# Performance work log

Measured on AMD Instinct MI355X. Metric: run time of the kernel, lower is better.

## Reference

```python
import jax, jax.numpy as jnp
import numpy as np

SLOPE = 0.2  # LeakyReLU negative slope

def _mlp2(x, w1, b1, w2, b2):
    h = jax.nn.leaky_relu(x @ w1 + b1, SLOPE)
    return h @ w2 + b2

def setup_inputs() -> dict:
    key = jax.random.key(0)
    ks = jax.random.split(key, 16)
    B, N, T, A, H = 8, 512, 8, 16, 64
    D = T * A  # node_dim * timestep = 128
    s = 0.1
    return {
        "nodes": jax.random.normal(ks[0], (B, N, T, A), dtype=jnp.float32),
        "edges": jax.random.randint(ks[1], (B, N, N), 0, 2),
        "self_w1": jax.random.normal(ks[2], (D, H), dtype=jnp.float32) * s,
        "self_b1": jnp.zeros((H,), jnp.float32),
        "self_w2": jax.random.normal(ks[3], (H, H), dtype=jnp.float32) * s,
        "self_b2": jnp.zeros((H,), jnp.float32),
        "nb_w1": jax.random.normal(ks[4], (D, H), dtype=jnp.float32) * s,
        "nb_b1": jnp.zeros((H,), jnp.float32),
        "nb_w2": jax.random.normal(ks[5], (H, H), dtype=jnp.float32) * s,
        "nb_b2": jnp.zeros((H,), jnp.float32),
        "comb_w1": jax.random.normal(ks[6], (2 * H, H), dtype=jnp.float32) * s,
        "comb_b1": jnp.zeros((H,), jnp.float32),
        "comb_w2": jax.random.normal(ks[7], (H, 1), dtype=jnp.float32) * s,
        "comb_b2": jnp.zeros((1,), jnp.float32),
    }

def reference(nodes, edges, self_w1, self_b1, self_w2, self_b2,
              nb_w1, nb_b1, nb_w2, nb_b2,
              comb_w1, comb_b1, comb_w2, comb_b2):
    B, N = nodes.shape[0], nodes.shape[1]
    H = self_w2.shape[1]
    x = nodes.reshape(B, N, -1)                       # [B,N,D]
    self_e = _mlp2(x, self_w1, self_b1, self_w2, self_b2)  # [B,N,H]
    nb_e = _mlp2(x, nb_w1, nb_b1, nb_w2, nb_b2)            # [B,N,H]

    # combine_mlp(cat(self_i, nb_j)) scores; split fc1 to avoid [B,N,N,2H]
    w1_s, w1_n = comb_w1[:H], comb_w1[H:]
    pre = (jnp.einsum('bih,hk->bik', self_e, w1_s)[:, :, None, :]
           + jnp.einsum('bjh,hk->bjk', nb_e, w1_n)[:, None, :, :]
           + comb_b1)                                  # [B,N,N,H] (i=target, j=neighbor)
    scores = (jax.nn.leaky_relu(pre, SLOPE) @ comb_w2)[..., 0] + comb_b2[0]  # [B,N,N]

    # mask[b,i,j] = edges[b,j,i] != 0 and i != j
    mask = (jnp.swapaxes(edges, 1, 2) != 0) & (~jnp.eye(N, dtype=bool))
    neg = jnp.finfo(scores.dtype).min
    weights = jax.nn.softmax(jnp.where(mask, scores, neg), axis=-1)
    weights = jnp.where(mask, weights, 0.0)

    agg = jnp.einsum('bij,bjh->bih', weights, nb_e)    # weighted neighbor sum
    has_nb = mask.any(-1)                              # nodes w/o neighbors stay zero
    return jnp.where(has_nb[..., None], agg + self_e, 0.0)
```

## Files before the change

kernel.cpp:

```cpp
#include <hip/hip_runtime.h>
#include <float.h>

typedef __attribute__((ext_vector_type(8))) short short8;
typedef __attribute__((ext_vector_type(4))) float f32x4;

#define SLOPE 0.2f

__device__ __forceinline__ float leaky(float x) { return fmaxf(x, SLOPE * x); }

__device__ __forceinline__ unsigned short f2bf(float f) {
  unsigned u = __float_as_uint(f);
  return (unsigned short)((u + 0x7FFFu + ((u >> 16) & 1u)) >> 16);
}

__global__ __launch_bounds__(64) void wprep(
    const float* __restrict__ self_w1, const float* __restrict__ self_w2,
    const float* __restrict__ nb_w1,   const float* __restrict__ nb_w2,
    const float* __restrict__ comb_w1,
    unsigned short* __restrict__ wf)
{
  const int frag = blockIdx.x;
  const int lane = threadIdx.x;
  const int p = frag >> 5, fl = frag & 31;
  const float* src;
  int nt, kb;
  if (fl < 16)      { src = p ? nb_w1 : self_w1; nt = fl >> 2;        kb = fl & 3; }
  else if (fl < 24) { src = p ? nb_w2 : self_w2; nt = (fl - 16) >> 1; kb = (fl - 16) & 1; }
  else              { src = comb_w1 + p * 4096;  nt = (fl - 24) >> 1; kb = (fl - 24) & 1; }
  const int n = nt * 16 + (lane & 15);
  const int k0 = kb * 32 + (lane >> 4) * 8;
  short8 pk;
  #pragma unroll
  for (int j = 0; j < 8; ++j) pk[j] = (short)f2bf(src[(k0 + j) * 64 + n]);
  *(short8*)(wf + ((size_t)(frag * 64 + lane)) * 8) = pk;
}

__global__ __launch_bounds__(64) void mlp(
    const float* __restrict__ nodes,
    const float* __restrict__ self_b1, const float* __restrict__ self_b2,
    const float* __restrict__ nb_b1,   const float* __restrict__ nb_b2,
    const float* __restrict__ comb_b1, const float* __restrict__ comb_w2,
    const float* __restrict__ comb_b2,
    const unsigned short* __restrict__ wf,
    float* __restrict__ self_e, float* __restrict__ ss, float* __restrict__ sn,
    float* __restrict__ sP, float* __restrict__ sQ,
    unsigned short* __restrict__ nbT)
{
  __shared__ float tile[16][68];

  const int lane = threadIdx.x;
  const int arow = lane & 15, agrp = lane >> 4;
  const int node0 = blockIdx.x * 16;
  const int b = node0 >> 9, jloc = node0 & 511;

  short8 xa[4];
  {
    const float* xrow = nodes + ((size_t)(node0 + arow)) * 128 + agrp * 8;
    #pragma unroll
    for (int kb = 0; kb < 4; ++kb) {
      float v[8];
      *(float4*)&v[0] = *(const float4*)(xrow + kb * 32);
      *(float4*)&v[4] = *(const float4*)(xrow + kb * 32 + 4);
      #pragma unroll
      for (int j = 0; j < 8; ++j) xa[kb][j] = (short)f2bf(v[j]);
    }
  }

  float w2vn[4], cb1v[4];
  #pragma unroll
  for (int nt = 0; nt < 4; ++nt) {
    w2vn[nt] = comb_w2[nt * 16 + arow];
    cb1v[nt] = comb_b1[nt * 16 + arow];
  }
  const float cb2 = comb_b2[0];

  for (int p = 0; p < 2; ++p) {
    const float* b1 = p ? nb_b1 : self_b1;
    const float* b2 = p ? nb_b2 : self_b2;
    const unsigned short* wfp = wf + (size_t)p * 32 * 64 * 8;

    short8 w1f[16], w2f[8], cwf[8];
    #pragma unroll
    for (int i = 0; i < 16; ++i)
      w1f[i] = *(const short8*)(wfp + ((size_t)(i * 64 + lane)) * 8);
    #pragma unroll
    for (int i = 0; i < 8; ++i)
      w2f[i] = *(const short8*)(wfp + ((size_t)((16 + i) * 64 + lane)) * 8);
    #pragma unroll
    for (int i = 0; i < 8; ++i)
      cwf[i] = *(const short8*)(wfp + ((size_t)((24 + i) * 64 + lane)) * 8);

    f32x4 acc[4];
    #pragma unroll
    for (int nt = 0; nt < 4; ++nt) acc[nt] = (f32x4){0.f, 0.f, 0.f, 0.f};
    #pragma unroll
    for (int kb = 0; kb < 4; ++kb)
      #pragma unroll
      for (int nt = 0; nt < 4; ++nt)
        acc[nt] = __builtin_amdgcn_mfma_f32_16x16x32_bf16(xa[kb], w1f[nt * 4 + kb], acc[nt], 0, 0, 0);
    #pragma unroll
    for (int nt = 0; nt < 4; ++nt) {
      const float bv = b1[nt * 16 + arow];
      #pragma unroll
      for (int r = 0; r < 4; ++r)
        tile[agrp * 4 + r][nt * 16 + arow] = leaky(acc[nt][r] + bv);
    }

    short8 ha[2];
    #pragma unroll
    for (int kb = 0; kb < 2; ++kb) {
      float v[8];
      *(float4*)&v[0] = *(const float4*)&tile[arow][kb * 32 + agrp * 8];
      *(float4*)&v[4] = *(const float4*)&tile[arow][kb * 32 + agrp * 8 + 4];
      #pragma unroll
      for (int j = 0; j < 8; ++j) ha[kb][j] = (short)f2bf(v[j]);
    }

    #pragma unroll
    for (int nt = 0; nt < 4; ++nt) acc[nt] = (f32x4){0.f, 0.f, 0.f, 0.f};
    #pragma unroll
    for (int kb = 0; kb < 2; ++kb)
      #pragma unroll
      for (int nt = 0; nt < 4; ++nt)
        acc[nt] = __builtin_amdgcn_mfma_f32_16x16x32_bf16(ha[kb], w2f[nt * 2 + kb], acc[nt], 0, 0, 0);
    #pragma unroll
    for (int nt = 0; nt < 4; ++nt) {
      const float bv = b2[nt * 16 + arow];
      #pragma unroll
      for (int r = 0; r < 4; ++r) {
        const float ev = acc[nt][r] + bv;
        tile[agrp * 4 + r][nt * 16 + arow] = ev;
        if (p == 0)
          self_e[((size_t)(node0 + agrp * 4 + r)) * 64 + nt * 16 + arow] = ev;
      }
    }

    short8 ea[2];
    #pragma unroll
    for (int kb = 0; kb < 2; ++kb) {
      float v[8];
      *(float4*)&v[0] = *(const float4*)&tile[arow][kb * 32 + agrp * 8];
      *(float4*)&v[4] = *(const float4*)&tile[arow][kb * 32 + agrp * 8 + 4];
      #pragma unroll
      for (int j = 0; j < 8; ++j) ea[kb][j] = (short)f2bf(v[j]);
    }

    if (p == 1) {
      #pragma unroll
      for (int g = 0; g < 2; ++g) {
        short8 pk;
        #pragma unroll
        for (int jj = 0; jj < 8; ++jj)
          pk[jj] = (short)f2bf(tile[g * 8 + jj][lane]);
        *(short8*)(nbT + (size_t)b * 32768 + ((size_t)((jloc >> 3) + g)) * 512 + lane * 8) = pk;
      }
    }

    #pragma unroll
    for (int nt = 0; nt < 4; ++nt) acc[nt] = (f32x4){0.f, 0.f, 0.f, 0.f};
    #pragma unroll
    for (int kb = 0; kb < 2; ++kb)
      #pragma unroll
      for (int nt = 0; nt < 4; ++nt)
        acc[nt] = __builtin_amdgcn_mfma_f32_16x16x32_bf16(ea[kb], cwf[nt * 2 + kb], acc[nt], 0, 0, 0);

    float* so = p ? sn : ss;
    float t[4] = {0.f, 0.f, 0.f, 0.f};
    #pragma unroll
    for (int nt = 0; nt < 4; ++nt) {
      #pragma unroll
      for (int r = 0; r < 4; ++r) {
        const float sv = acc[nt][r] + (p ? 0.f : cb1v[nt]);
        so[((size_t)(node0 + agrp * 4 + r)) * 64 + nt * 16 + arow] = sv;
        t[r] += w2vn[nt] * sv;
      }
    }
    #pragma unroll
    for (int r = 0; r < 4; ++r) {
      #pragma unroll
      for (int off = 1; off < 16; off <<= 1) t[r] += __shfl_xor(t[r], off);
    }
    if (arow == 0) {
      float* po = p ? sQ : sP;
      const float add = p ? 0.f : cb2;
      #pragma unroll
      for (int r = 0; r < 4; ++r)
        po[node0 + agrp * 4 + r] = 0.6f * t[r] + add;
    }
  }
}

__global__ __launch_bounds__(512) void gat_attn(
    const int* __restrict__ edges,
    const float* __restrict__ comb_w2,
    const float* __restrict__ self_e,
    const float* __restrict__ ss, const float* __restrict__ sn,
    const float* __restrict__ sP, const float* __restrict__ sQ,
    const unsigned short* __restrict__ nbT,
    float* __restrict__ out)
{
  __shared__ __align__(16) float sn_sh[2][64][68];
  __shared__ __align__(16) unsigned short P_sh[16][520];
  __shared__ __align__(16) float red_sh[4][64][4];
  __shared__ unsigned short jm_sh[512];
  __shared__ float f_sh[16];

  const int tid = threadIdx.x, lane = tid & 63, wv = tid >> 6;
  const int b = blockIdx.x & 7, it = blockIdx.x >> 3;
  const int i0 = it * 16;
  const size_t nodeb = (size_t)b * 512;

  const int ra = wv * 2, rb = ra + 1;
  const int ia = i0 + ra, ib = ia + 1;

  const int* ebp = edges + ((size_t)(nodeb + tid)) * 512 + i0;
  const int4 ev0 = *(const int4*)(ebp + 0);
  const int4 ev1 = *(const int4*)(ebp + 4);
  const int4 ev2 = *(const int4*)(ebp + 8);
  const int4 ev3 = *(const int4*)(ebp + 12);

  float4 w2p[16], sa0[16], sa1[16];
  {
    const float4* w2v = (const float4*)comb_w2;
    const float4* s0 = (const float4*)(ss + (nodeb + ia) * 64);
    const float4* s1 = (const float4*)(ss + (nodeb + ib) * 64);
    #pragma unroll
    for (int q = 0; q < 16; ++q) {
      float4 w = w2v[q];
      w2p[q] = make_float4(0.4f * w.x, 0.4f * w.y, 0.4f * w.z, 0.4f * w.w);
      sa0[q] = s0[q];
      sa1[q] = s1[q];
    }
  }
  const float sPa = sP[nodeb + ia], sPb = sP[nodeb + ib];
  float sQv[8];
  #pragma unroll
  for (int jt = 0; jt < 8; ++jt) sQv[jt] = sQ[nodeb + jt * 64 + lane];

  {
    unsigned mj = 0;
    mj |= (ev0.x != 0 ? 1u : 0u) << 0;  mj |= (ev0.y != 0 ? 1u : 0u) << 1;
    mj |= (ev0.z != 0 ? 1u : 0u) << 2;  mj |= (ev0.w != 0 ? 1u : 0u) << 3;
    mj |= (ev1.x != 0 ? 1u : 0u) << 4;  mj |= (ev1.y != 0 ? 1u : 0u) << 5;
    mj |= (ev1.z != 0 ? 1u : 0u) << 6;  mj |= (ev1.w != 0 ? 1u : 0u) << 7;
    mj |= (ev2.x != 0 ? 1u : 0u) << 8;  mj |= (ev2.y != 0 ? 1u : 0u) << 9;
    mj |= (ev2.z != 0 ? 1u : 0u) << 10; mj |= (ev2.w != 0 ? 1u : 0u) << 11;
    mj |= (ev3.x != 0 ? 1u : 0u) << 12; mj |= (ev3.y != 0 ? 1u : 0u) << 13;
    mj |= (ev3.z != 0 ? 1u : 0u) << 14; mj |= (ev3.w != 0 ? 1u : 0u) << 15;
    const int d = tid - i0;
    if (d >= 0 && d < 16) mj &= ~(1u << d);
    jm_sh[tid] = (unsigned short)mj;
  }

  const int str = tid >> 4, stc = (tid & 15) * 4;
  const int str2 = (tid + 512) >> 4, stc2 = ((tid + 512) & 15) * 4;
  float4 st0, st1;
  {
    const float4* src = (const float4*)(sn + nodeb * 64);
    st0 = src[tid];
    st1 = src[tid + 512];
  }

  float msc0[8], msc1[8];
  int cur = 0;
  for (int jt = 0; jt < 8; ++jt) {
    *(float4*)&sn_sh[cur][str][stc] = st0;
    *(float4*)&sn_sh[cur][str2][stc2] = st1;
    if (jt < 7) {
      const float4* src = (const float4*)(sn + (nodeb + (jt + 1) * 64) * 64);
      st0 = src[tid];
      st1 = src[tid + 512];
    }
    __syncthreads();

    float acc0 = 0.f, acc1 = 0.f;
    #pragma unroll
    for (int q = 0; q < 16; ++q) {
      float4 v = *(const float4*)&sn_sh[cur][lane][q * 4];
      float4 w = w2p[q];
      float4 A = sa0[q];
      float4 Bv = sa1[q];
      acc0 += w.x * fabsf(A.x + v.x) + w.y * fabsf(A.y + v.y)
            + w.z * fabsf(A.z + v.z) + w.w * fabsf(A.w + v.w);
      acc1 += w.x * fabsf(Bv.x + v.x) + w.y * fabsf(Bv.y + v.y)
            + w.z * fabsf(Bv.z + v.z) + w.w * fabsf(Bv.w + v.w);
    }
    const unsigned mj = jm_sh[jt * 64 + lane];
    msc0[jt] = ((mj >> ra) & 1u) ? acc0 + sPa + sQv[jt] : -FLT_MAX;
    msc1[jt] = ((mj >> rb) & 1u) ? acc1 + sPb + sQv[jt] : -FLT_MAX;
    cur ^= 1;
  }

  float m0 = msc0[0], m1 = msc1[0];
  #pragma unroll
  for (int jt = 1; jt < 8; ++jt) {
    m0 = fmaxf(m0, msc0[jt]);
    m1 = fmaxf(m1, msc1[jt]);
  }
  #pragma unroll
  for (int off = 32; off; off >>= 1) {
    m0 = fmaxf(m0, __shfl_xor(m0, off));
    m1 = fmaxf(m1, __shfl_xor(m1, off));
  }

  float s0 = 0.f, s1 = 0.f;
  #pragma unroll
  for (int jt = 0; jt < 8; ++jt) {
    const float e0 = __expf(msc0[jt] - m0);
    const float e1 = __expf(msc1[jt] - m1);
    P_sh[ra][jt * 64 + lane] = f2bf(e0);
    P_sh[rb][jt * 64 + lane] = f2bf(e1);
    s0 += e0;
    s1 += e1;
  }
  #pragma unroll
  for (int off = 32; off; off >>= 1) {
    s0 += __shfl_xor(s0, off);
    s1 += __shfl_xor(s1, off);
  }
  if (lane == 0) {
    f_sh[ra] = (m0 > -1e37f) ? 1.0f / s0 : 0.0f;
    f_sh[rb] = (m1 > -1e37f) ? 1.0f / s1 : 0.0f;
  }
  __syncthreads();

  const int nt = wv & 3, kh = wv >> 2;
  const int arow = lane & 15, agrp = lane >> 4;
  const int bcol = nt * 16 + (lane & 15);
  const unsigned short* nb3 = nbT + (size_t)b * 32768 + bcol * 8;

  f32x4 C = {0.f, 0.f, 0.f, 0.f};
  #pragma unroll
  for (int ks = 0; ks < 8; ++ks) {
    const int jb = kh * 256 + ks * 32 + agrp * 8;
    short8 afr = *(const short8*)&P_sh[arow][jb];
    short8 bfr = *(const short8*)(nb3 + (size_t)jb * 64);
    C = __builtin_amdgcn_mfma_f32_16x16x32_bf16(afr, bfr, C, 0, 0, 0);
  }
  if (kh == 1) *(f32x4*)&red_sh[wv - 4][lane][0] = C;
  __syncthreads();
  if (kh == 0) {
    f32x4 P = *(const f32x4*)&red_sh[wv][lane][0];
    #pragma unroll
    for (int r = 0; r < 4; ++r) {
      const int rg = agrp * 4 + r;
      const float f = f_sh[rg];
      const size_t adr = (nodeb + i0 + rg) * 64 + bcol;
      const float val = (C[r] + P[r]) * f + self_e[adr];
      out[adr] = (f > 0.f) ? val : 0.f;
    }
  }
}

extern "C" void kernel_launch(void* const* d_in, const int* in_sizes, int n_in,
                              void* d_out, int out_size, void* d_ws, size_t ws_size,
                              hipStream_t stream) {
  const float* nodes   = (const float*)d_in[0];
  const int*   edges   = (const int*)  d_in[1];
  const float* self_w1 = (const float*)d_in[2];
  const float* self_b1 = (const float*)d_in[3];
  const float* self_w2 = (const float*)d_in[4];
  const float* self_b2 = (const float*)d_in[5];
  const float* nb_w1   = (const float*)d_in[6];
  const float* nb_b1   = (const float*)d_in[7];
  const float* nb_w2   = (const float*)d_in[8];
  const float* nb_b2   = (const float*)d_in[9];
  const float* comb_w1 = (const float*)d_in[10];
  const float* comb_b1 = (const float*)d_in[11];
  const float* comb_w2 = (const float*)d_in[12];
  const float* comb_b2 = (const float*)d_in[13];

  float* ws     = (float*)d_ws;
  float* self_e = ws;
  float* ss     = ws + 262144;
  float* sn     = ws + 524288;
  float* sP     = ws + 786432;
  float* sQ     = ws + 790528;
  unsigned short* nbT = (unsigned short*)(ws + 794624);
  unsigned short* wf  = (unsigned short*)(ws + 925696);

  wprep<<<64, 64, 0, stream>>>(self_w1, self_w2, nb_w1, nb_w2, comb_w1, wf);

  mlp<<<256, 64, 0, stream>>>(
      nodes, self_b1, self_b2, nb_b1, nb_b2, comb_b1, comb_w2, comb_b2,
      wf, self_e, ss, sn, sP, sQ, nbT);

  gat_attn<<<256, 512, 0, stream>>>(
      edges, comb_w2, self_e, ss, sn, sP, sQ, nbT, (float*)d_out);
}
```

Before: 34.62 us.

## Pack transposed edge mask into bitmasks in a prep kernel merged with weight prep

Adds a preprocessing pass, folded into the weight-prep kernel, that reads the int32 edge matrix through a shared-memory transpose and uses ballots to write 64-bit per-target neighbor bitmasks. The attention kernel then reads compact bitmasks instead of strided int4 edge loads, and drops the shared mask array. This moves the edge read off the attention kernel's critical path and runs it ahead of the MLP kernel. The cost is an extra global write and read of the mask plus a larger prep kernel, whose edge blocks do 8 sequential tile iterations.

```diff
diff --git a/kernel.cpp b/kernel.cpp
--- a/kernel.cpp
+++ b/kernel.cpp
@@ -13,26 +13,53 @@
   return (unsigned short)((u + 0x7FFFu + ((u >> 16) & 1u)) >> 16);
 }
 
-__global__ __launch_bounds__(64) void wprep(
+__global__ __launch_bounds__(256) void pre(
+    const int* __restrict__ edges,
     const float* __restrict__ self_w1, const float* __restrict__ self_w2,
     const float* __restrict__ nb_w1,   const float* __restrict__ nb_w2,
     const float* __restrict__ comb_w1,
-    unsigned short* __restrict__ wf)
+    unsigned short* __restrict__ wf, unsigned long long* __restrict__ ep)
 {
-  const int frag = blockIdx.x;
-  const int lane = threadIdx.x;
-  const int p = frag >> 5, fl = frag & 31;
-  const float* src;
-  int nt, kb;
-  if (fl < 16)      { src = p ? nb_w1 : self_w1; nt = fl >> 2;        kb = fl & 3; }
-  else if (fl < 24) { src = p ? nb_w2 : self_w2; nt = (fl - 16) >> 1; kb = (fl - 16) & 1; }
-  else              { src = comb_w1 + p * 4096;  nt = (fl - 24) >> 1; kb = (fl - 24) & 1; }
-  const int n = nt * 16 + (lane & 15);
-  const int k0 = kb * 32 + (lane >> 4) * 8;
-  short8 pk;
-  #pragma unroll
-  for (int j = 0; j < 8; ++j) pk[j] = (short)f2bf(src[(k0 + j) * 64 + n]);
-  *(short8*)(wf + ((size_t)(frag * 64 + lane)) * 8) = pk;
+  __shared__ int t_sh[64][65];
+  const int tid = threadIdx.x, lane = tid & 63, wv = tid >> 6;
+
+  if (blockIdx.x >= 64) {
+    const int frag = (blockIdx.x - 64) * 4 + wv;
+    const int p = frag >> 5, fl = frag & 31;
+    const float* src;
+    int nt, kb;
+    if (fl < 16)      { src = p ? nb_w1 : self_w1; nt = fl >> 2;        kb = fl & 3; }
+    else if (fl < 24) { src = p ? nb_w2 : self_w2; nt = (fl - 16) >> 1; kb = (fl - 16) & 1; }
+    else              { src = comb_w1 + p * 4096;  nt = (fl - 24) >> 1; kb = (fl - 24) & 1; }
+    const int n = nt * 16 + (lane & 15);
+    const int k0 = kb * 32 + (lane >> 4) * 8;
+    short8 pk;
+    #pragma unroll
+    for (int j = 0; j < 8; ++j) pk[j] = (short)f2bf(src[(k0 + j) * 64 + n]);
+    *(short8*)(wf + ((size_t)(frag * 64 + lane)) * 8) = pk;
+    return;
+  }
+
+  const int blk = blockIdx.x;
+  const int b = blk >> 3, it = blk & 7;
+  const int i0 = it * 64;
+  for (int jt = 0; jt < 8; ++jt) {
+    #pragma unroll
+    for (int r = 0; r < 4; ++r) {
+      const int idx = r * 256 + tid;
+      const int jr = idx >> 4, i4 = (idx & 15) * 4;
+      *(int4*)&t_sh[jr][i4] =
+          *(const int4*)&edges[((size_t)(b * 512 + jt * 64 + jr)) * 512 + i0 + i4];
+    }
+    __syncthreads();
+    #pragma unroll
+    for (int u = 0; u < 16; ++u) {
+      const int ic = wv * 16 + u;
+      const unsigned long long m = __ballot(t_sh[lane][ic] != 0);
+      if (lane == 0) ep[((size_t)(b * 512 + i0 + ic)) * 8 + jt] = m;
+    }
+    __syncthreads();
+  }
 }
 
 __global__ __launch_bounds__(64) void mlp(
@@ -191,7 +218,7 @@
 }
 
 __global__ __launch_bounds__(512) void gat_attn(
-    const int* __restrict__ edges,
+    const unsigned long long* __restrict__ ep,
     const float* __restrict__ comb_w2,
     const float* __restrict__ self_e,
     const float* __restrict__ ss, const float* __restrict__ sn,
@@ -202,7 +229,6 @@
   __shared__ __align__(16) float sn_sh[2][64][68];
   __shared__ __align__(16) unsigned short P_sh[16][520];
   __shared__ __align__(16) float red_sh[4][64][4];
-  __shared__ unsigned short jm_sh[512];
   __shared__ float f_sh[16];
 
   const int tid = threadIdx.x, lane = tid & 63, wv = tid >> 6;
@@ -213,11 +239,24 @@
   const int ra = wv * 2, rb = ra + 1;
   const int ia = i0 + ra, ib = ia + 1;
 
-  const int* ebp = edges + ((size_t)(nodeb + tid)) * 512 + i0;
-  const int4 ev0 = *(const int4*)(ebp + 0);
-  const int4 ev1 = *(const int4*)(ebp + 4);
-  const int4 ev2 = *(const int4*)(ebp + 8);
-  const int4 ev3 = *(const int4*)(ebp + 12);
+  unsigned em0 = 0, em1 = 0;
+  float sQv[8];
+  {
+    const unsigned long long* e0 = ep + (nodeb + ia) * 8;
+    const unsigned long long* e1 = ep + (nodeb + ib) * 8;
+    #pragma unroll
+    for (int jt = 0; jt < 8; ++jt) {
+      em0 |= (unsigned)((e0[jt] >> lane) & 1ull) << jt;
+      em1 |= (unsigned)((e1[jt] >> lane) & 1ull) << jt;
+      sQv[jt] = sQ[nodeb + jt * 64 + lane];
+    }
+  }
+  {
+    const int d0 = ia - lane;
+    if (d0 >= 0 && (d0 & 63) == 0) em0 &= ~(1u << (d0 >> 6));
+    const int d1 = ib - lane;
+    if (d1 >= 0 && (d1 & 63) == 0) em1 &= ~(1u << (d1 >> 6));
+  }
 
   float4 w2p[16], sa0[16], sa1[16];
   {
@@ -233,24 +272,6 @@
     }
   }
   const float sPa = sP[nodeb + ia], sPb = sP[nodeb + ib];
-  float sQv[8];
-  #pragma unroll
-  for (int jt = 0; jt < 8; ++jt) sQv[jt] = sQ[nodeb + jt * 64 + lane];
-
-  {
-    unsigned mj = 0;
-    mj |= (ev0.x != 0 ? 1u : 0u) << 0;  mj |= (ev0.y != 0 ? 1u : 0u) << 1;
-    mj |= (ev0.z != 0 ? 1u : 0u) << 2;  mj |= (ev0.w != 0 ? 1u : 0u) << 3;
-    mj |= (ev1.x != 0 ? 1u : 0u) << 4;  mj |= (ev1.y != 0 ? 1u : 0u) << 5;
-    mj |= (ev1.z != 0 ? 1u : 0u) << 6;  mj |= (ev1.w != 0 ? 1u : 0u) << 7;
-    mj |= (ev2.x != 0 ? 1u : 0u) << 8;  mj |= (ev2.y != 0 ? 1u : 0u) << 9;
-    mj |= (ev2.z != 0 ? 1u : 0u) << 10; mj |= (ev2.w != 0 ? 1u : 0u) << 11;
-    mj |= (ev3.x != 0 ? 1u : 0u) << 12; mj |= (ev3.y != 0 ? 1u : 0u) << 13;
-    mj |= (ev3.z != 0 ? 1u : 0u) << 14; mj |= (ev3.w != 0 ? 1u : 0u) << 15;
-    const int d = tid - i0;
-    if (d >= 0 && d < 16) mj &= ~(1u << d);
-    jm_sh[tid] = (unsigned short)mj;
-  }
 
   const int str = tid >> 4, stc = (tid & 15) * 4;
   const int str2 = (tid + 512) >> 4, stc2 = ((tid + 512) & 15) * 4;
@@ -285,9 +306,8 @@
       acc1 += w.x * fabsf(Bv.x + v.x) + w.y * fabsf(Bv.y + v.y)
             + w.z * fabsf(Bv.z + v.z) + w.w * fabsf(Bv.w + v.w);
     }
-    const unsigned mj = jm_sh[jt * 64 + lane];
-    msc0[jt] = ((mj >> ra) & 1u) ? acc0 + sPa + sQv[jt] : -FLT_MAX;
-    msc1[jt] = ((mj >> rb) & 1u) ? acc1 + sPb + sQv[jt] : -FLT_MAX;
+    msc0[jt] = ((em0 >> jt) & 1u) ? acc0 + sPa + sQv[jt] : -FLT_MAX;
+    msc1[jt] = ((em1 >> jt) & 1u) ? acc1 + sPb + sQv[jt] : -FLT_MAX;
     cur ^= 1;
   }
 
@@ -378,13 +398,15 @@
   float* sQ     = ws + 790528;
   unsigned short* nbT = (unsigned short*)(ws + 794624);
   unsigned short* wf  = (unsigned short*)(ws + 925696);
-
-  wprep<<<64, 64, 0, stream>>>(self_w1, self_w2, nb_w1, nb_w2, comb_w1, wf);
+  unsigned long long* ep = (unsigned long long*)(ws + 942080);
+
+  pre<<<80, 256, 0, stream>>>(edges, self_w1, self_w2, nb_w1, nb_w2, comb_w1,
+                              wf, ep);
 
   mlp<<<256, 64, 0, stream>>>(
       nodes, self_b1, self_b2, nb_b1, nb_b2, comb_b1, comb_w2, comb_b2,
       wf, self_e, ss, sn, sP, sQ, nbT);
 
   gat_attn<<<256, 512, 0, stream>>>(
-      edges, comb_w2, self_e, ss, sn, sP, sQ, nbT, (float*)d_out);
+      ep, comb_w2, self_e, ss, sn, sP, sQ, nbT, (float*)d_out);
 }
```

Measured after the change: 39.46 us. 14.0% more time.

## Split attention blocks to 8 target rows with 256 threads over 512 blocks

Applied to the files above, without the earlier changes.

The attention kernel now handles 8 target rows per block with 4 waves, giving 512 blocks instead of 256 blocks of 16 rows and 8 waves. The MFMA aggregation runs the full K=512 range per wave, which removes the cross-wave shared-memory reduction and its extra barrier. Unused P rows are zero-padded so the 16-row MFMA stays valid, and half its output is discarded. In exchange, each block stages the full neighbor score tile for only half as many rows, doubling total sn traffic, and MFMA work is half wasted.

```diff
diff --git a/kernel.cpp b/kernel.cpp
--- a/kernel.cpp
+++ b/kernel.cpp
@@ -190,7 +190,7 @@
   }
 }
 
-__global__ __launch_bounds__(512) void gat_attn(
+__global__ __launch_bounds__(256) void gat_attn(
     const int* __restrict__ edges,
     const float* __restrict__ comb_w2,
     const float* __restrict__ self_e,
@@ -201,23 +201,43 @@
 {
   __shared__ __align__(16) float sn_sh[2][64][68];
   __shared__ __align__(16) unsigned short P_sh[16][520];
-  __shared__ __align__(16) float red_sh[4][64][4];
-  __shared__ unsigned short jm_sh[512];
-  __shared__ float f_sh[16];
+  __shared__ unsigned char jm_sh[512];
+  __shared__ float f_sh[8];
 
   const int tid = threadIdx.x, lane = tid & 63, wv = tid >> 6;
   const int b = blockIdx.x & 7, it = blockIdx.x >> 3;
-  const int i0 = it * 16;
+  const int i0 = it * 8;
   const size_t nodeb = (size_t)b * 512;
 
   const int ra = wv * 2, rb = ra + 1;
   const int ia = i0 + ra, ib = ia + 1;
 
-  const int* ebp = edges + ((size_t)(nodeb + tid)) * 512 + i0;
-  const int4 ev0 = *(const int4*)(ebp + 0);
-  const int4 ev1 = *(const int4*)(ebp + 4);
-  const int4 ev2 = *(const int4*)(ebp + 8);
-  const int4 ev3 = *(const int4*)(ebp + 12);
+  {
+    uint4* pz = (uint4*)&P_sh[8][0];
+    for (int k = tid; k < 520; k += 256) pz[k] = make_uint4(0, 0, 0, 0);
+  }
+
+  {
+    const int* e0 = edges + ((size_t)(nodeb + tid)) * 512 + i0;
+    const int* e1 = edges + ((size_t)(nodeb + tid + 256)) * 512 + i0;
+    int4 a0 = *(const int4*)e0, a1 = *(const int4*)(e0 + 4);
+    int4 c0 = *(const int4*)e1, c1 = *(const int4*)(e1 + 4);
+    unsigned mA = 0, mB = 0;
+    mA |= (a0.x != 0 ? 1u : 0u) << 0; mA |= (a0.y != 0 ? 1u : 0u) << 1;
+    mA |= (a0.z != 0 ? 1u : 0u) << 2; mA |= (a0.w != 0 ? 1u : 0u) << 3;
+    mA |= (a1.x != 0 ? 1u : 0u) << 4; mA |= (a1.y != 0 ? 1u : 0u) << 5;
+    mA |= (a1.z != 0 ? 1u : 0u) << 6; mA |= (a1.w != 0 ? 1u : 0u) << 7;
+    mB |= (c0.x != 0 ? 1u : 0u) << 0; mB |= (c0.y != 0 ? 1u : 0u) << 1;
+    mB |= (c0.z != 0 ? 1u : 0u) << 2; mB |= (c0.w != 0 ? 1u : 0u) << 3;
+    mB |= (c1.x != 0 ? 1u : 0u) << 4; mB |= (c1.y != 0 ? 1u : 0u) << 5;
+    mB |= (c1.z != 0 ? 1u : 0u) << 6; mB |= (c1.w != 0 ? 1u : 0u) << 7;
+    const int dA = tid - i0;
+    if (dA >= 0 && dA < 8) mA &= ~(1u << dA);
+    const int dB = tid + 256 - i0;
+    if (dB >= 0 && dB < 8) mB &= ~(1u << dB);
+    jm_sh[tid] = (unsigned char)mA;
+    jm_sh[tid + 256] = (unsigned char)mB;
+  }
 
   float4 w2p[16], sa0[16], sa1[16];
   {
@@ -237,39 +257,25 @@
   #pragma unroll
   for (int jt = 0; jt < 8; ++jt) sQv[jt] = sQ[nodeb + jt * 64 + lane];
 
-  {
-    unsigned mj = 0;
-    mj |= (ev0.x != 0 ? 1u : 0u) << 0;  mj |= (ev0.y != 0 ? 1u : 0u) << 1;
-    mj |= (ev0.z != 0 ? 1u : 0u) << 2;  mj |= (ev0.w != 0 ? 1u : 0u) << 3;
-    mj |= (ev1.x != 0 ? 1u : 0u) << 4;  mj |= (ev1.y != 0 ? 1u : 0u) << 5;
-    mj |= (ev1.z != 0 ? 1u : 0u) << 6;  mj |= (ev1.w != 0 ? 1u : 0u) << 7;
-    mj |= (ev2.x != 0 ? 1u : 0u) << 8;  mj |= (ev2.y != 0 ? 1u : 0u) << 9;
-    mj |= (ev2.z != 0 ? 1u : 0u) << 10; mj |= (ev2.w != 0 ? 1u : 0u) << 11;
-    mj |= (ev3.x != 0 ? 1u : 0u) << 12; mj |= (ev3.y != 0 ? 1u : 0u) << 13;
-    mj |= (ev3.z != 0 ? 1u : 0u) << 14; mj |= (ev3.w != 0 ? 1u : 0u) << 15;
-    const int d = tid - i0;
-    if (d >= 0 && d < 16) mj &= ~(1u << d);
-    jm_sh[tid] = (unsigned short)mj;
-  }
-
-  const int str = tid >> 4, stc = (tid & 15) * 4;
-  const int str2 = (tid + 512) >> 4, stc2 = ((tid + 512) & 15) * 4;
-  float4 st0, st1;
+  float4 st[4];
   {
     const float4* src = (const float4*)(sn + nodeb * 64);
-    st0 = src[tid];
-    st1 = src[tid + 512];
+    #pragma unroll
+    for (int u = 0; u < 4; ++u) st[u] = src[u * 256 + tid];
   }
 
   float msc0[8], msc1[8];
   int cur = 0;
   for (int jt = 0; jt < 8; ++jt) {
-    *(float4*)&sn_sh[cur][str][stc] = st0;
-    *(float4*)&sn_sh[cur][str2][stc2] = st1;
+    #pragma unroll
+    for (int u = 0; u < 4; ++u) {
+      const int t = u * 256 + tid;
+      *(float4*)&sn_sh[cur][t >> 4][(t & 15) * 4] = st[u];
+    }
     if (jt < 7) {
       const float4* src = (const float4*)(sn + (nodeb + (jt + 1) * 64) * 64);
-      st0 = src[tid];
-      st1 = src[tid + 512];
+      #pragma unroll
+      for (int u = 0; u < 4; ++u) st[u] = src[u * 256 + tid];
     }
     __syncthreads();
 
@@ -324,30 +330,29 @@
   }
   __syncthreads();
 
-  const int nt = wv & 3, kh = wv >> 2;
+  const int nt = wv;
   const int arow = lane & 15, agrp = lane >> 4;
   const int bcol = nt * 16 + (lane & 15);
   const unsigned short* nb3 = nbT + (size_t)b * 32768 + bcol * 8;
 
   f32x4 C = {0.f, 0.f, 0.f, 0.f};
   #pragma unroll
-  for (int ks = 0; ks < 8; ++ks) {
-    const int jb = kh * 256 + ks * 32 + agrp * 8;
+  for (int ks = 0; ks < 16; ++ks) {
+    const int jb = ks * 32 + agrp * 8;
     short8 afr = *(const short8*)&P_sh[arow][jb];
     short8 bfr = *(const short8*)(nb3 + (size_t)jb * 64);
     C = __builtin_amdgcn_mfma_f32_16x16x32_bf16(afr, bfr, C, 0, 0, 0);
   }
-  if (kh == 1) *(f32x4*)&red_sh[wv - 4][lane][0] = C;
-  __syncthreads();
-  if (kh == 0) {
-    f32x4 P = *(const f32x4*)&red_sh[wv][lane][0];
+  {
     #pragma unroll
     for (int r = 0; r < 4; ++r) {
       const int rg = agrp * 4 + r;
-      const float f = f_sh[rg];
-      const size_t adr = (nodeb + i0 + rg) * 64 + bcol;
-      const float val = (C[r] + P[r]) * f + self_e[adr];
-      out[adr] = (f > 0.f) ? val : 0.f;
+      if (rg < 8) {
+        const float f = f_sh[rg];
+        const size_t adr = (nodeb + i0 + rg) * 64 + bcol;
+        const float val = C[r] * f + self_e[adr];
+        out[adr] = (f > 0.f) ? val : 0.f;
+      }
     }
   }
 }
@@ -385,6 +390,6 @@
       nodes, self_b1, self_b2, nb_b1, nb_b2, comb_b1, comb_w2, comb_b2,
       wf, self_e, ss, sn, sP, sQ, nbT);
 
-  gat_attn<<<256, 512, 0, stream>>>(
+  gat_attn<<<512, 256, 0, stream>>>(
       edges, comb_w2, self_e, ss, sn, sP, sQ, nbT, (float*)d_out);
 }
```

Result: slower. 63.45 us (+83.2%).

## Halve target rows per attention block to double grid and occupancy

Applied to the files above, without the earlier changes.

Each gat_attn block now handles 8 target nodes instead of 16, one row per wave, so the launch grows from 256 to 512 blocks and fills more of the GPU's compute units. Each wave's register state shrinks (one row of self-scores instead of two), and launch_bounds asks for 4 blocks per SM. The upper half of the P tile is zeroed so the 16-row MFMA still works, and only 8 output rows are written. The cost is that every block re-reads the neighbour-embedding stream and the nbT B-operand for half as many rows, roughly doubling that traffic, and half of each MFMA is wasted on zero rows.

```diff
diff --git a/kernel.cpp b/kernel.cpp
--- a/kernel.cpp
+++ b/kernel.cpp
@@ -190,7 +190,7 @@
   }
 }
 
-__global__ __launch_bounds__(512) void gat_attn(
+__global__ __launch_bounds__(512, 4) void gat_attn(
     const int* __restrict__ edges,
     const float* __restrict__ comb_w2,
     const float* __restrict__ self_e,
@@ -202,55 +202,50 @@
   __shared__ __align__(16) float sn_sh[2][64][68];
   __shared__ __align__(16) unsigned short P_sh[16][520];
   __shared__ __align__(16) float red_sh[4][64][4];
-  __shared__ unsigned short jm_sh[512];
-  __shared__ float f_sh[16];
+  __shared__ unsigned char jm_sh[512];
+  __shared__ float f_sh[8];
 
   const int tid = threadIdx.x, lane = tid & 63, wv = tid >> 6;
   const int b = blockIdx.x & 7, it = blockIdx.x >> 3;
-  const int i0 = it * 16;
+  const int i0 = it * 8;
   const size_t nodeb = (size_t)b * 512;
 
-  const int ra = wv * 2, rb = ra + 1;
-  const int ia = i0 + ra, ib = ia + 1;
-
-  const int* ebp = edges + ((size_t)(nodeb + tid)) * 512 + i0;
-  const int4 ev0 = *(const int4*)(ebp + 0);
-  const int4 ev1 = *(const int4*)(ebp + 4);
-  const int4 ev2 = *(const int4*)(ebp + 8);
-  const int4 ev3 = *(const int4*)(ebp + 12);
-
-  float4 w2p[16], sa0[16], sa1[16];
+  const int row = wv;
+  const int ia = i0 + row;
+
+  {
+    uint4* pz = (uint4*)&P_sh[8][0];
+    for (int k = tid; k < 520; k += 512) pz[k] = make_uint4(0, 0, 0, 0);
+  }
+
+  {
+    const int* e0 = edges + ((size_t)(nodeb + tid)) * 512 + i0;
+    int4 a0 = *(const int4*)e0, a1 = *(const int4*)(e0 + 4);
+    unsigned mA = 0;
+    mA |= (a0.x != 0 ? 1u : 0u) << 0; mA |= (a0.y != 0 ? 1u : 0u) << 1;
+    mA |= (a0.z != 0 ? 1u : 0u) << 2; mA |= (a0.w != 0 ? 1u : 0u) << 3;
+    mA |= (a1.x != 0 ? 1u : 0u) << 4; mA |= (a1.y != 0 ? 1u : 0u) << 5;
+    mA |= (a1.z != 0 ? 1u : 0u) << 6; mA |= (a1.w != 0 ? 1u : 0u) << 7;
+    const int d = tid - i0;
+    if (d >= 0 && d < 8) mA &= ~(1u << d);
+    jm_sh[tid] = (unsigned char)mA;
+  }
+
+  float4 w2p[16], sa[16];
   {
     const float4* w2v = (const float4*)comb_w2;
     const float4* s0 = (const float4*)(ss + (nodeb + ia) * 64);
-    const float4* s1 = (const float4*)(ss + (nodeb + ib) * 64);
     #pragma unroll
     for (int q = 0; q < 16; ++q) {
       float4 w = w2v[q];
       w2p[q] = make_float4(0.4f * w.x, 0.4f * w.y, 0.4f * w.z, 0.4f * w.w);
-      sa0[q] = s0[q];
-      sa1[q] = s1[q];
-    }
-  }
-  const float sPa = sP[nodeb + ia], sPb = sP[nodeb + ib];
+      sa[q] = s0[q];
+    }
+  }
+  const float sPa = sP[nodeb + ia];
   float sQv[8];
   #pragma unroll
   for (int jt = 0; jt < 8; ++jt) sQv[jt] = sQ[nodeb + jt * 64 + lane];
-
-  {
-    unsigned mj = 0;
-    mj |= (ev0.x != 0 ? 1u : 0u) << 0;  mj |= (ev0.y != 0 ? 1u : 0u) << 1;
-    mj |= (ev0.z != 0 ? 1u : 0u) << 2;  mj |= (ev0.w != 0 ? 1u : 0u) << 3;
-    mj |= (ev1.x != 0 ? 1u : 0u) << 4;  mj |= (ev1.y != 0 ? 1u : 0u) << 5;
-    mj |= (ev1.z != 0 ? 1u : 0u) << 6;  mj |= (ev1.w != 0 ? 1u : 0u) << 7;
-    mj |= (ev2.x != 0 ? 1u : 0u) << 8;  mj |= (ev2.y != 0 ? 1u : 0u) << 9;
-    mj |= (ev2.z != 0 ? 1u : 0u) << 10; mj |= (ev2.w != 0 ? 1u : 0u) << 11;
-    mj |= (ev3.x != 0 ? 1u : 0u) << 12; mj |= (ev3.y != 0 ? 1u : 0u) << 13;
-    mj |= (ev3.z != 0 ? 1u : 0u) << 14; mj |= (ev3.w != 0 ? 1u : 0u) << 15;
-    const int d = tid - i0;
-    if (d >= 0 && d < 16) mj &= ~(1u << d);
-    jm_sh[tid] = (unsigned short)mj;
-  }
 
   const int str = tid >> 4, stc = (tid & 15) * 4;
   const int str2 = (tid + 512) >> 4, stc2 = ((tid + 512) & 15) * 4;
@@ -261,7 +256,7 @@
     st1 = src[tid + 512];
   }
 
-  float msc0[8], msc1[8];
+  float msc[8];
   int cur = 0;
   for (int jt = 0; jt < 8; ++jt) {
     *(float4*)&sn_sh[cur][str][stc] = st0;
@@ -278,50 +273,31 @@
     for (int q = 0; q < 16; ++q) {
       float4 v = *(const float4*)&sn_sh[cur][lane][q * 4];
       float4 w = w2p[q];
-      float4 A = sa0[q];
-      float4 Bv = sa1[q];
-      acc0 += w.x * fabsf(A.x + v.x) + w.y * fabsf(A.y + v.y)
-            + w.z * fabsf(A.z + v.z) + w.w * fabsf(A.w + v.w);
-      acc1 += w.x * fabsf(Bv.x + v.x) + w.y * fabsf(Bv.y + v.y)
-            + w.z * fabsf(Bv.z + v.z) + w.w * fabsf(Bv.w + v.w);
+      float4 A = sa[q];
+      acc0 += w.x * fabsf(A.x + v.x) + w.y * fabsf(A.y + v.y);
+      acc1 += w.z * fabsf(A.z + v.z) + w.w * fabsf(A.w + v.w);
     }
     const unsigned mj = jm_sh[jt * 64 + lane];
-    msc0[jt] = ((mj >> ra) & 1u) ? acc0 + sPa + sQv[jt] : -FLT_MAX;
-    msc1[jt] = ((mj >> rb) & 1u) ? acc1 + sPb + sQv[jt] : -FLT_MAX;
+    msc[jt] = ((mj >> row) & 1u) ? acc0 + acc1 + sPa + sQv[jt] : -FLT_MAX;
     cur ^= 1;
   }
 
-  float m0 = msc0[0], m1 = msc1[0];
-  #pragma unroll
-  for (int jt = 1; jt < 8; ++jt) {
-    m0 = fmaxf(m0, msc0[jt]);
-    m1 = fmaxf(m1, msc1[jt]);
-  }
-  #pragma unroll
-  for (int off = 32; off; off >>= 1) {
-    m0 = fmaxf(m0, __shfl_xor(m0, off));
-    m1 = fmaxf(m1, __shfl_xor(m1, off));
-  }
-
-  float s0 = 0.f, s1 = 0.f;
+  float m0 = msc[0];
+  #pragma unroll
+  for (int jt = 1; jt < 8; ++jt) m0 = fmaxf(m0, msc[jt]);
+  #pragma unroll
+  for (int off = 32; off; off >>= 1) m0 = fmaxf(m0, __shfl_xor(m0, off));
+
+  float s0 = 0.f;
   #pragma unroll
   for (int jt = 0; jt < 8; ++jt) {
-    const float e0 = __expf(msc0[jt] - m0);
-    const float e1 = __expf(msc1[jt] - m1);
-    P_sh[ra][jt * 64 + lane] = f2bf(e0);
-    P_sh[rb][jt * 64 + lane] = f2bf(e1);
+    const float e0 = __expf(msc[jt] - m0);
+    P_sh[row][jt * 64 + lane] = f2bf(e0);
     s0 += e0;
-    s1 += e1;
-  }
-  #pragma unroll
-  for (int off = 32; off; off >>= 1) {
-    s0 += __shfl_xor(s0, off);
-    s1 += __shfl_xor(s1, off);
-  }
-  if (lane == 0) {
-    f_sh[ra] = (m0 > -1e37f) ? 1.0f / s0 : 0.0f;
-    f_sh[rb] = (m1 > -1e37f) ? 1.0f / s1 : 0.0f;
-  }
+  }
+  #pragma unroll
+  for (int off = 32; off; off >>= 1) s0 += __shfl_xor(s0, off);
+  if (lane == 0) f_sh[row] = (m0 > -1e37f) ? 1.0f / s0 : 0.0f;
   __syncthreads();
 
   const int nt = wv & 3, kh = wv >> 2;
@@ -344,10 +320,12 @@
     #pragma unroll
     for (int r = 0; r < 4; ++r) {
       const int rg = agrp * 4 + r;
-      const float f = f_sh[rg];
-      const size_t adr = (nodeb + i0 + rg) * 64 + bcol;
-      const float val = (C[r] + P[r]) * f + self_e[adr];
-      out[adr] = (f > 0.f) ? val : 0.f;
+      if (rg < 8) {
+        const float f = f_sh[rg];
+        const size_t adr = (nodeb + i0 + rg) * 64 + bcol;
+        const float val = (C[r] + P[r]) * f + self_e[adr];
+        out[adr] = (f > 0.f) ? val : 0.f;
+      }
     }
   }
 }
@@ -385,6 +363,6 @@
       nodes, self_b1, self_b2, nb_b1, nb_b2, comb_b1, comb_w2, comb_b2,
       wf, self_e, ss, sn, sP, sQ, nbT);
 
-  gat_attn<<<256, 512, 0, stream>>>(
+  gat_attn<<<512, 512, 0, stream>>>(
       edges, comb_w2, self_e, ss, sn, sP, sQ, nbT, (float*)d_out);
 }
```

New measurement: 98.63 us. 2.85x slower.
